# Kernel optimization log

Hardware: AMD Instinct MI355X
Metric: run time of the kernel (lower is better)

## Reference

```python
import jax, jax.numpy as jnp
import numpy as np
from math import pi

N = 256        # in_features == out_features
BATCH = 131072


def givens_orthogonal(angles, n):
    """Build an n x n orthogonal matrix as the ordered product of Givens
    rotations G(i, j, theta_k) over pairs i < j in lexicographic order.
    Each rotation mixes rows i and j; applied sequentially via lax.scan."""
    ii, jj = np.triu_indices(n, 1)  # static pair order, len = n*(n-1)//2
    ii = jnp.asarray(ii, dtype=jnp.int32)
    jj = jnp.asarray(jj, dtype=jnp.int32)

    def body(M, t):
        i, j, th = t
        c, s = jnp.cos(th), jnp.sin(th)
        ri, rj = M[i], M[j]
        M = M.at[i].set(c * ri - s * rj)
        M = M.at[j].set(s * ri + c * rj)
        return M, None

    M0 = jnp.eye(n, dtype=angles.dtype)
    M, _ = jax.lax.scan(body, M0, (ii, jj, angles))
    return M


def setup_inputs() -> dict:
    key = jax.random.key(0)
    k1, k2, k3 = jax.random.split(key, 3)
    n_ang = N * (N - 1) // 2  # 32640
    return {
        "x": jax.random.normal(k1, (BATCH, N), dtype=jnp.float32),
        "Uweight": jax.random.uniform(k2, (n_ang,), minval=-pi / 2, maxval=pi / 2, dtype=jnp.float32),
        "Vweight": jax.random.uniform(k3, (n_ang,), minval=-pi / 2, maxval=pi / 2, dtype=jnp.float32),
        "Sweight": jnp.ones((N,), dtype=jnp.float32),
        "bias": jnp.zeros((N,), dtype=jnp.float32),
    }


def reference(x, Uweight, Vweight, Sweight, bias):
    # W = V @ diag(S) @ U^T  (SVD-parametrized weight, out x in)
    # y = x @ W^T + b = ((x @ U) * S) @ V^T + b   (square case in == out)
    U = givens_orthogonal(Uweight, N)  # (in, in) orthogonal
    V = givens_orthogonal(Vweight, N)  # (out, out) orthogonal
    return ((x @ U) * Sweight) @ V.T + bias
```

## Files before the change

kernel.cpp:

```cpp
#include <hip/hip_runtime.h>
#include <hip/hip_bf16.h>
#include <math.h>

#define NN 256
#define NSEG 32
#define MAT (NN*NN)

#define MATS0 0
#define MATS1 (MATS0 + 64*MAT)
#define WBT_OFF (MATS1 + 32*MAT)

static __device__ const int BD[NSEG+1] =
    {0,4,8,12,16,20,24,28,32,37,42,47,52,57,62,67,73,79,85,91,97,
     104,111,118,126,134,143,153,164,177,192,213,255};
#define CSL_CAP 1120

typedef __attribute__((ext_vector_type(8))) short short8;
typedef __attribute__((ext_vector_type(4))) float f32x4;

__device__ __forceinline__ short f2bf(float f) {
    __hip_bfloat16 h = __float2bfloat16(f);
    return *reinterpret_cast<short*>(&h);
}

#define BAR() do {                                              \
    asm volatile("s_waitcnt lgkmcnt(0)" ::: "memory");          \
    __builtin_amdgcn_s_barrier();                               \
    asm volatile("" ::: "memory");                              \
} while (0)

__global__ __launch_bounds__(64) void k_build(const float* __restrict__ au,
                                              const float* __restrict__ av,
                                              float* __restrict__ mats) {
    int b = blockIdx.x;
    int matid = b >> 7;
    int seg   = (b >> 2) & 31;
    int chunk = b & 3;
    int t = threadIdx.x;
    int c0 = chunk * 64;
    int i0 = BD[seg], i1 = BD[seg+1];
    float* outp = mats + (matid * NSEG + seg) * MAT;

    if (c0 + 64 <= i0) {
        for (int id = t; id < 4096; id += 64) {
            int row = id >> 4, c4 = (id & 15) * 4;
            float4 v = {0.f,0.f,0.f,0.f};
            int d = row - (c0 + c4);
            if (d >= 0 && d < 4) ((float*)&v)[d] = 1.0f;
            *(float4*)(outp + row*NN + c0 + c4) = v;
        }
        return;
    }

    __shared__ float M[NN * 64];
    __shared__ float2 csl[CSL_CAP];

    int kbase = 255*i0 - (i0*(i0-1))/2;
    int kend  = 255*i1 - (i1*(i1-1))/2;
    int nrot  = kend - kbase;
    const float* ang = (matid ? av : au) + kbase;
    for (int idx = t; idx < nrot; idx += 64) {
        float s, c;
        sincosf(ang[idx], &s, &c);
        float2 v = {c, s};
        csl[idx] = v;
    }

    int MR = NN - i0;
    for (int rr = 0; rr < MR; ++rr)
        M[rr*64 + t] = (i0 + rr == c0 + t) ? 1.0f : 0.0f;
    __syncthreads();

    for (int i = i0; i < i1; ++i) {
        int jstart = (i + 1 > c0) ? (i + 1) : c0;
        int kl = 255*i - (i*(i-1))/2 + (jstart - i - 1) - kbase;
        float ri = M[(i - i0)*64 + t];
        int j = jstart;
        int ng = (NN - jstart) >> 3;

        float2 cb[8]; float rj[8];
        if (ng > 0) {
#pragma unroll
            for (int u = 0; u < 8; ++u) cb[u] = csl[kl + u];
#pragma unroll
            for (int u = 0; u < 8; ++u) rj[u] = M[(j - i0 + u)*64 + t];
        }
        for (int g = 0; g < ng; ++g) {
            float2 cn[8]; float rn[8];
            if (g + 1 < ng) {
#pragma unroll
                for (int u = 0; u < 8; ++u) cn[u] = csl[kl + 8 + u];
#pragma unroll
                for (int u = 0; u < 8; ++u) rn[u] = M[(j + 8 - i0 + u)*64 + t];
            }
#pragma unroll
            for (int u = 0; u < 8; ++u) {
                float wv = cb[u].y*ri + cb[u].x*rj[u];
                ri       = cb[u].x*ri - cb[u].y*rj[u];
                M[(j - i0 + u)*64 + t] = wv;
            }
#pragma unroll
            for (int u = 0; u < 8; ++u) { cb[u] = cn[u]; rj[u] = rn[u]; }
            j += 8; kl += 8;
        }
        int rem = NN - j;
        if (rem > 0) {
            float2 cc[7]; float r7[7];
#pragma unroll
            for (int u = 0; u < 7; ++u)
                if (u < rem) { cc[u] = csl[kl + u];
                               r7[u] = M[(j - i0 + u)*64 + t]; }
#pragma unroll
            for (int u = 0; u < 7; ++u)
                if (u < rem) {
                    float wv = cc[u].y*ri + cc[u].x*r7[u];
                    ri       = cc[u].x*ri - cc[u].y*r7[u];
                    M[(j - i0 + u)*64 + t] = wv;
                }
        }
        M[(i - i0)*64 + t] = ri;
    }
    __syncthreads();

    for (int id = t; id < 4096; id += 64) {
        int row = id >> 4, c4 = (id & 15) * 4;
        float4 v;
        if (row < i0) {
            v = make_float4(0.f,0.f,0.f,0.f);
            int d = row - (c0 + c4);
            if (d >= 0 && d < 4) ((float*)&v)[d] = 1.0f;
        } else {
            v = *(const float4*)&M[(row - i0)*64 + c4];
        }
        *(float4*)(outp + row*NN + c0 + c4) = v;
    }
}

__device__ __forceinline__ void fold_body(const float* __restrict__ in,
                                          float* __restrict__ out,
                                          int nOut, int lg, int span,
                                          int b, int t) {
    int np2 = 2 * nOut;
    int m    = b & (np2 - 1);
    int tile = b >> lg;
    int side = (m >= nOut) ? 1 : 0;
    int q = m - side * nOut;
    const float* A = in + (side*np2 + 2*q + 1) * MAT;
    const float* B = in + (side*np2 + 2*q) * MAT;
    float* C = out + m * MAT;
    int i0A = BD[q * span + (span >> 1)];
    int r0 = (tile >> 2) * 64, c0 = (tile & 3) * 64;

    if (r0 + 64 <= i0A) {
#pragma unroll
        for (int u = 0; u < 4; ++u) {
            int id = u*256 + t;
            int rr = id >> 4, cc = (id & 15) * 4;
            *(float4*)(C + (r0+rr)*NN + c0 + cc) =
                *(const float4*)(B + (r0+rr)*NN + c0 + cc);
        }
        return;
    }

    int kstart = ((r0 < i0A) ? r0 : i0A) & ~31;
    int nt = (NN - kstart) >> 5;

    __shared__ float Ast[2][32][68];
    __shared__ float Bs [2][32][68];
    int tx = t & 15, ty = t >> 4;
    int arow = t >> 3, ak4 = t & 7;
    int bkr = t >> 4, bc4 = t & 15;

    float acc[4][4] = {};
    f32x4 pa0, pa1, pb0, pb1;
    {
        int kt = kstart;
        pa0 = *(const f32x4*)(A + (r0 + arow     )*NN + kt + ak4*4);
        pa1 = *(const f32x4*)(A + (r0 + arow + 32)*NN + kt + ak4*4);
        pb0 = *(const f32x4*)(B + (kt + bkr      )*NN + c0 + bc4*4);
        pb1 = *(const f32x4*)(B + (kt + bkr + 16 )*NN + c0 + bc4*4);
    }
    for (int it = 0; it < nt; ++it) {
        int cur = it & 1;
#pragma unroll
        for (int jj = 0; jj < 4; ++jj) {
            Ast[cur][ak4*4 + jj][arow]      = pa0[jj];
            Ast[cur][ak4*4 + jj][arow + 32] = pa1[jj];
        }
        *(f32x4*)&Bs[cur][bkr     ][bc4*4] = pb0;
        *(f32x4*)&Bs[cur][bkr + 16][bc4*4] = pb1;
        if (it + 1 < nt) {
            int k2 = kstart + (it+1)*32;
            pa0 = *(const f32x4*)(A + (r0 + arow     )*NN + k2 + ak4*4);
            pa1 = *(const f32x4*)(A + (r0 + arow + 32)*NN + k2 + ak4*4);
            pb0 = *(const f32x4*)(B + (k2 + bkr      )*NN + c0 + bc4*4);
            pb1 = *(const f32x4*)(B + (k2 + bkr + 16 )*NN + c0 + bc4*4);
        }
        BAR();
#pragma unroll 8
        for (int kk = 0; kk < 32; ++kk) {
            f32x4 a4 = *(const f32x4*)&Ast[cur][kk][ty*4];
            f32x4 b4 = *(const f32x4*)&Bs [cur][kk][tx*4];
#pragma unroll
            for (int rr = 0; rr < 4; ++rr)
#pragma unroll
                for (int cc = 0; cc < 4; ++cc)
                    acc[rr][cc] = fmaf(a4[rr], b4[cc], acc[rr][cc]);
        }
    }
#pragma unroll
    for (int rr = 0; rr < 4; ++rr) {
        float4 o = {acc[rr][0], acc[rr][1], acc[rr][2], acc[rr][3]};
        *(float4*)(C + (r0 + ty*4 + rr)*NN + c0 + tx*4) = o;
    }
}

__global__ __launch_bounds__(256) void k_fold1(const float* in, float* out)
{ fold_body(in, out, 16, 5,  2, blockIdx.x, threadIdx.x); }
__global__ __launch_bounds__(256) void k_fold2(const float* in, float* out)
{ fold_body(in, out,  8, 4,  4, blockIdx.x, threadIdx.x); }
__global__ __launch_bounds__(256) void k_fold3(const float* in, float* out)
{ fold_body(in, out,  4, 3,  8, blockIdx.x, threadIdx.x); }
__global__ __launch_bounds__(256) void k_fold4(const float* in, float* out)
{ fold_body(in, out,  2, 2, 16, blockIdx.x, threadIdx.x); }
__global__ __launch_bounds__(256) void k_fold5(const float* in, float* out)
{ fold_body(in, out,  1, 1, 32, blockIdx.x, threadIdx.x); }

__global__ __launch_bounds__(256) void k_wmatT(const float* __restrict__ U,
                                               const float* __restrict__ V,
                                               const float* __restrict__ S,
                                               unsigned short* __restrict__ Wbt) {
    int b = blockIdx.x;
    int n0 = (b >> 4) * 16, i0 = (b & 15) * 16;
    int t = threadIdx.x, ti = t & 15, tn = t >> 4;
    __shared__ float Us[16][260];
    __shared__ float Vs[16][260];
    {
        int rr = t >> 4, cc = (t & 15) * 16;
#pragma unroll
        for (int q = 0; q < 4; ++q) {
            float4 u = *(const float4*)(U + (i0+rr)*NN + cc + q*4);
            float4 s = *(const float4*)(S + cc + q*4);
            u.x *= s.x; u.y *= s.y; u.z *= s.z; u.w *= s.w;
            *(float4*)&Us[rr][cc+q*4] = u;
            *(float4*)&Vs[rr][cc+q*4] = *(const float4*)(V + (n0+rr)*NN + cc + q*4);
        }
    }
    __syncthreads();
    float acc = 0.f;
#pragma unroll 8
    for (int k4 = 0; k4 < 64; ++k4) {
        float4 uu = *(const float4*)&Us[ti][k4*4];
        float4 vv = *(const float4*)&Vs[tn][k4*4];
        acc += uu.x*vv.x + uu.y*vv.y + uu.z*vv.z + uu.w*vv.w;
    }
    Wbt[(n0+tn)*NN + (i0+ti)] = (unsigned short)f2bf(acc);
}

__global__ __launch_bounds__(512, 4) void k_mm(const float* __restrict__ x,
                                               const unsigned short* __restrict__ Wbt,
                                               const float* __restrict__ bias,
                                               float* __restrict__ out) {
    int t = threadIdx.x;
    int w = t >> 6, l = t & 63, l15 = l & 15, lg = l >> 4;
    int n0 = w * 32;

    __shared__ unsigned short Xs[2][8 * 512];

    long rowbase = (long)blockIdx.x * 256;
    int r = t & 15, m = t >> 4;
    int ksb = m >> 2;
    int lidx = r + 16 * (m & 3);

    const float* s0 = x + (rowbase + r) * NN + 8*m;
    float4 f0 = *(const float4*)(s0);
    float4 f1 = *(const float4*)(s0 + 4);

    short8 bfrag[2][8];
#pragma unroll
    for (int nt = 0; nt < 2; ++nt) {
        const unsigned short* wrow = Wbt + (n0 + nt*16 + l15) * NN + lg * 8;
#pragma unroll
        for (int ks = 0; ks < 8; ++ks)
            bfrag[nt][ks] = *(const short8*)(wrow + ks * 32);
    }
    asm volatile("" : "+v"(bfrag[0][0]), "+v"(bfrag[0][1]),
                      "+v"(bfrag[0][2]), "+v"(bfrag[0][3]),
                      "+v"(bfrag[0][4]), "+v"(bfrag[0][5]),
                      "+v"(bfrag[0][6]), "+v"(bfrag[0][7]));
    asm volatile("" : "+v"(bfrag[1][0]), "+v"(bfrag[1][1]),
                      "+v"(bfrag[1][2]), "+v"(bfrag[1][3]),
                      "+v"(bfrag[1][4]), "+v"(bfrag[1][5]),
                      "+v"(bfrag[1][6]), "+v"(bfrag[1][7]));

    float b0 = bias[n0 + l15];
    float b1 = bias[n0 + 16 + l15];

    for (int it = 0; it < 16; ++it) {
        int cur = it & 1;
        short8 h;
        h[0]=f2bf(f0.x); h[1]=f2bf(f0.y); h[2]=f2bf(f0.z); h[3]=f2bf(f0.w);
        h[4]=f2bf(f1.x); h[5]=f2bf(f1.y); h[6]=f2bf(f1.z); h[7]=f2bf(f1.w);
        *(short8*)&Xs[cur][ksb*512 + lidx*8] = h;
        if (it < 15) {
            const float* sn = x + (rowbase + (it+1)*16 + r) * NN + 8*m;
            f0 = *(const float4*)(sn);
            f1 = *(const float4*)(sn + 4);
        }
        BAR();

        f32x4 acc0 = {0.f,0.f,0.f,0.f}, acc1 = {0.f,0.f,0.f,0.f};
#pragma unroll
        for (int ks = 0; ks < 8; ++ks) {
            short8 af = *(const short8*)&Xs[cur][ks*512 + l*8];
            acc0 = __builtin_amdgcn_mfma_f32_16x16x32_bf16(af, bfrag[0][ks], acc0, 0, 0, 0);
            acc1 = __builtin_amdgcn_mfma_f32_16x16x32_bf16(af, bfrag[1][ks], acc1, 0, 0, 0);
        }
        float* op = out + (rowbase + it*16 + lg*4) * NN + n0 + l15;
#pragma unroll
        for (int rr = 0; rr < 4; ++rr) {
            op[rr * NN]      = acc0[rr] + b0;
            op[rr * NN + 16] = acc1[rr] + b1;
        }
    }
}

extern "C" void kernel_launch(void* const* d_in, const int* in_sizes, int n_in,
                              void* d_out, int out_size, void* d_ws, size_t ws_size,
                              hipStream_t stream) {
    const float* x    = (const float*)d_in[0];
    const float* Uw   = (const float*)d_in[1];
    const float* Vw   = (const float*)d_in[2];
    const float* Sw   = (const float*)d_in[3];
    const float* bias = (const float*)d_in[4];
    float* out = (float*)d_out;
    float* ws  = (float*)d_ws;

    k_build<<<256, 64, 0, stream>>>(Uw, Vw, ws + MATS0);
    k_fold1<<<16*32, 256, 0, stream>>>(ws + MATS0, ws + MATS1);
    k_fold2<<<16*16, 256, 0, stream>>>(ws + MATS1, ws + MATS0);
    k_fold3<<<16* 8, 256, 0, stream>>>(ws + MATS0, ws + MATS1);
    k_fold4<<<16* 4, 256, 0, stream>>>(ws + MATS1, ws + MATS0);
    k_fold5<<<16* 2, 256, 0, stream>>>(ws + MATS0, ws + MATS1);
    k_wmatT<<<256, 256, 0, stream>>>(ws + MATS1, ws + MATS1 + MAT, Sw,
                                     (unsigned short*)(ws + WBT_OFF));
    k_mm<<<512, 512, 0, stream>>>(x, (unsigned short*)(ws + WBT_OFF), bias, out);
}
```

Before: 192.9 us.

## Block Givens rotations four rows at a time and use nontemporal output stores

The segment-building kernel now processes four consecutive pivot rows together. It first applies the rotations among those rows in registers, then streams each target row once through all four rotations, which cuts LDS reads and writes of M roughly fourfold. The GEMM kernel drops the asm register-pinning barriers on the B fragments and writes output with nontemporal stores to avoid polluting cache. The gains are fewer LDS round trips in the serial rotation chain and lower cache pressure on output, at the cost of more registers and more complex indexing.

```diff
diff --git a/kernel.cpp b/kernel.cpp
--- a/kernel.cpp
+++ b/kernel.cpp
@@ -65,60 +65,102 @@
         float2 v = {c, s};
         csl[idx] = v;
     }
-
     int MR = NN - i0;
     for (int rr = 0; rr < MR; ++rr)
         M[rr*64 + t] = (i0 + rr == c0 + t) ? 1.0f : 0.0f;
     __syncthreads();
 
-    for (int i = i0; i < i1; ++i) {
-        int jstart = (i + 1 > c0) ? (i + 1) : c0;
-        int kl = 255*i - (i*(i-1))/2 + (jstart - i - 1) - kbase;
-        float ri = M[(i - i0)*64 + t];
-        int j = jstart;
-        int ng = (NN - jstart) >> 3;
-
-        float2 cb[8]; float rj[8];
-        if (ng > 0) {
-#pragma unroll
-            for (int u = 0; u < 8; ++u) cb[u] = csl[kl + u];
-#pragma unroll
-            for (int u = 0; u < 8; ++u) rj[u] = M[(j - i0 + u)*64 + t];
-        }
-        for (int g = 0; g < ng; ++g) {
-            float2 cn[8]; float rn[8];
-            if (g + 1 < ng) {
-#pragma unroll
-                for (int u = 0; u < 8; ++u) cn[u] = csl[kl + 8 + u];
-#pragma unroll
-                for (int u = 0; u < 8; ++u) rn[u] = M[(j + 8 - i0 + u)*64 + t];
+    int i = i0;
+    while (i < i1) {
+        int bs = i1 - i; if (bs > 4) bs = 4;
+        float r[4];
+#pragma unroll
+        for (int k = 0; k < 4; ++k)
+            if (k < bs) r[k] = M[(i + k - i0)*64 + t];
+
+#pragma unroll
+        for (int a = 0; a < 3; ++a)
+#pragma unroll
+            for (int b2 = a + 1; b2 < 4; ++b2)
+                if (b2 < bs && i + b2 >= c0) {
+                    int aa = i + a;
+                    int idx = 255*aa - (aa*(aa-1))/2 + (b2 - a - 1) - kbase;
+                    float2 cs = csl[idx];
+                    float wv = cs.y*r[a] + cs.x*r[b2];
+                    r[a]  = cs.x*r[a] - cs.y*r[b2];
+                    r[b2] = wv;
+                }
+
+        int jblk = i + bs; if (jblk < c0) jblk = c0;
+        int base[4];
+#pragma unroll
+        for (int k = 0; k < 4; ++k) {
+            int a = i + k;
+            base[k] = 255*a - (a*(a-1))/2 - a - 1 - kbase;
+        }
+
+        int j = jblk;
+        int ngr = (NN - jblk) >> 2;
+        float rjc[4]; float2 csc[4][4];
+        if (ngr > 0) {
+#pragma unroll
+            for (int u = 0; u < 4; ++u) rjc[u] = M[(j + u - i0)*64 + t];
+#pragma unroll
+            for (int k = 0; k < 4; ++k)
+                if (k < bs)
+#pragma unroll
+                    for (int u = 0; u < 4; ++u)
+                        csc[k][u] = csl[base[k] + j + u];
+        }
+        for (int g = 0; g < ngr; ++g) {
+            float rjn[4]; float2 csn[4][4];
+            if (g + 1 < ngr) {
+#pragma unroll
+                for (int u = 0; u < 4; ++u) rjn[u] = M[(j + 4 + u - i0)*64 + t];
+#pragma unroll
+                for (int k = 0; k < 4; ++k)
+                    if (k < bs)
+#pragma unroll
+                        for (int u = 0; u < 4; ++u)
+                            csn[k][u] = csl[base[k] + j + 4 + u];
             }
 #pragma unroll
-            for (int u = 0; u < 8; ++u) {
-                float wv = cb[u].y*ri + cb[u].x*rj[u];
-                ri       = cb[u].x*ri - cb[u].y*rj[u];
-                M[(j - i0 + u)*64 + t] = wv;
+            for (int u = 0; u < 4; ++u) {
+                float rj = rjc[u];
+#pragma unroll
+                for (int k = 0; k < 4; ++k)
+                    if (k < bs) {
+                        float2 cs = csc[k][u];
+                        float wv = cs.y*r[k] + cs.x*rj;
+                        r[k] = cs.x*r[k] - cs.y*rj;
+                        rj = wv;
+                    }
+                M[(j + u - i0)*64 + t] = rj;
             }
 #pragma unroll
-            for (int u = 0; u < 8; ++u) { cb[u] = cn[u]; rj[u] = rn[u]; }
-            j += 8; kl += 8;
-        }
-        int rem = NN - j;
-        if (rem > 0) {
-            float2 cc[7]; float r7[7];
-#pragma unroll
-            for (int u = 0; u < 7; ++u)
-                if (u < rem) { cc[u] = csl[kl + u];
-                               r7[u] = M[(j - i0 + u)*64 + t]; }
-#pragma unroll
-            for (int u = 0; u < 7; ++u)
-                if (u < rem) {
-                    float wv = cc[u].y*ri + cc[u].x*r7[u];
-                    ri       = cc[u].x*ri - cc[u].y*r7[u];
-                    M[(j - i0 + u)*64 + t] = wv;
+            for (int u = 0; u < 4; ++u) rjc[u] = rjn[u];
+#pragma unroll
+            for (int k = 0; k < 4; ++k)
+#pragma unroll
+                for (int u = 0; u < 4; ++u) csc[k][u] = csn[k][u];
+            j += 4;
+        }
+        for (; j < NN; ++j) {
+            float rj = M[(j - i0)*64 + t];
+#pragma unroll
+            for (int k = 0; k < 4; ++k)
+                if (k < bs) {
+                    float2 cs = csl[base[k] + j];
+                    float wv = cs.y*r[k] + cs.x*rj;
+                    r[k] = cs.x*r[k] - cs.y*rj;
+                    rj = wv;
                 }
-        }
-        M[(i - i0)*64 + t] = ri;
+            M[(j - i0)*64 + t] = rj;
+        }
+#pragma unroll
+        for (int k = 0; k < 4; ++k)
+            if (k < bs) M[(i + k - i0)*64 + t] = r[k];
+        i += bs;
     }
     __syncthreads();
 
@@ -284,15 +326,6 @@
         for (int ks = 0; ks < 8; ++ks)
             bfrag[nt][ks] = *(const short8*)(wrow + ks * 32);
     }
-    asm volatile("" : "+v"(bfrag[0][0]), "+v"(bfrag[0][1]),
-                      "+v"(bfrag[0][2]), "+v"(bfrag[0][3]),
-                      "+v"(bfrag[0][4]), "+v"(bfrag[0][5]),
-                      "+v"(bfrag[0][6]), "+v"(bfrag[0][7]));
-    asm volatile("" : "+v"(bfrag[1][0]), "+v"(bfrag[1][1]),
-                      "+v"(bfrag[1][2]), "+v"(bfrag[1][3]),
-                      "+v"(bfrag[1][4]), "+v"(bfrag[1][5]),
-                      "+v"(bfrag[1][6]), "+v"(bfrag[1][7]));
-
     float b0 = bias[n0 + l15];
     float b1 = bias[n0 + 16 + l15];
 
@@ -319,8 +352,8 @@
         float* op = out + (rowbase + it*16 + lg*4) * NN + n0 + l15;
 #pragma unroll
         for (int rr = 0; rr < 4; ++rr) {
-            op[rr * NN]      = acc0[rr] + b0;
-            op[rr * NN + 16] = acc1[rr] + b1;
+            __builtin_nontemporal_store(acc0[rr] + b0, op + rr * NN);
+            __builtin_nontemporal_store(acc1[rr] + b1, op + rr * NN + 16);
         }
     }
 }
```

After: 189.2 us, median of 3. About the same (-1.9%).
